# Performance work log

Measured on AMD Instinct MI355X. Metric: run time of the kernel, lower is better.

## Reference

```python
import jax, jax.numpy as jnp
import numpy as np

NUM_ANCHORS = 9  # 3 ratios * 3 sizes


def setup_inputs() -> dict:
    key = jax.random.key(0)
    k0, k1, k2, k3 = jax.random.split(key, 4)
    B, C, H, W = 4, 256, 200, 336
    resnet_features = jax.random.normal(k0, (B, C, H, W), dtype=jnp.float32)
    # 3x3 conv: C -> 512
    W1 = jax.random.normal(k1, (512, C, 3, 3), dtype=jnp.float32) * 0.02
    b1 = jnp.zeros((512,), dtype=jnp.float32)
    # 1x1 cls head: 512 -> 9*2
    Wc = jax.random.normal(k2, (NUM_ANCHORS * 2, 512), dtype=jnp.float32) * 0.02
    bc = jnp.zeros((NUM_ANCHORS * 2,), dtype=jnp.float32)
    # 1x1 bbox head: 512 -> 9*4
    Wb = jax.random.normal(k3, (NUM_ANCHORS * 4, 512), dtype=jnp.float32) * 0.02
    bb = jnp.zeros((NUM_ANCHORS * 4,), dtype=jnp.float32)
    return {"resnet_features": resnet_features, "W1": W1, "b1": b1,
            "Wc": Wc, "bc": bc, "Wb": Wb, "bb": bb}


def reference(resnet_features, W1, b1, Wc, bc, Wb, bb):
    B = resnet_features.shape[0]
    # conv3x3 + ReLU (padding=1 -> SAME)
    feat = jax.lax.conv_general_dilated(
        resnet_features, W1, window_strides=(1, 1), padding='SAME',
        dimension_numbers=('NCHW', 'OIHW', 'NCHW'))
    feat = jax.nn.relu(feat + b1[None, :, None, None])  # [B,512,H,W]
    # 1x1 conv heads as channel contractions
    cls = jnp.einsum('bchw,oc->bohw', feat, Wc) + bc[None, :, None, None]
    box = jnp.einsum('bchw,oc->bohw', feat, Wb) + bb[None, :, None, None]
    # permute(0,2,3,1).view(B,-1,2/4)
    anchor_cls_score = jnp.transpose(cls, (0, 2, 3, 1)).reshape(B, -1, 2)
    anchor_bboxdelta = jnp.transpose(box, (0, 2, 3, 1)).reshape(B, -1, 4)
    return anchor_cls_score, anchor_bboxdelta
```

## Files before the change

### kernel.cpp

```cpp
#include <hip/hip_runtime.h>
#include <hip/hip_bf16.h>
#include <stdint.h>

#define B_   4
#define C_   256
#define H_   200
#define W_   336
#define OC_  512
#define HP_  202
#define WP_  338
#define M_   (B_*H_*W_)
#define MTILES (M_/128)
#define OUT0_ (M_*18)
#define OUT_TOTAL_ (M_*54)

#define XP_ELEMS  ((size_t)B_*HP_*WP_*C_)
#define XP_BYTES  (XP_ELEMS*2)
#define W1T_ELEMS ((size_t)9*OC_*C_)
#define W1T_OFF   XP_BYTES
#define WHB_OFF   (W1T_OFF + W1T_ELEMS*2)

typedef unsigned short ushortT;
typedef __attribute__((ext_vector_type(8))) short bf16x8;
typedef __attribute__((ext_vector_type(4))) float f32x4;

static __device__ __forceinline__ ushortT f2bf(float x) {
    union { float f; uint32_t u; } v; v.f = x;
    uint32_t r = v.u + 0x7fff + ((v.u >> 16) & 1);
    return (ushortT)(r >> 16);
}

__global__ __launch_bounds__(256) void pad_transpose(const float* __restrict__ X,
                                                     ushortT* __restrict__ Xp) {
    int bid = blockIdx.x;
    int wc = bid % 6; int bh = bid / 6;
    int h = bh % H_;  int b = bh / H_;
    int w0 = wc * 64;
    int t = threadIdx.x;
    __shared__ ushortT tile[64 * 65];

    for (int c0 = 0; c0 < C_; c0 += 64) {
        if (c0) __syncthreads();
        int col  = t & 63;
        int rowb = t >> 6;
        #pragma unroll
        for (int rr = 0; rr < 16; ++rr) {
            int row = rowb * 16 + rr;
            int w = w0 + col;
            float val = 0.f;
            if (w < W_)
                val = X[(((size_t)(b*C_ + c0 + row))*H_ + h)*W_ + w];
            tile[row*65 + col] = f2bf(val);
        }
        __syncthreads();
        int pixel = t >> 2;
        int csub  = (t & 3) * 16;
        int w = w0 + pixel;
        if (w < W_) {
            union { ushortT u[16]; uint4 q[2]; } vals;
            #pragma unroll
            for (int j = 0; j < 16; ++j)
                vals.u[j] = tile[(csub + j)*65 + pixel];
            size_t dst = (((size_t)b*HP_ + (h+1))*WP_ + (w+1))*C_ + c0 + csub;
            *(uint4*)(Xp + dst)     = vals.q[0];
            *(uint4*)(Xp + dst + 8) = vals.q[1];
        }
    }
}

__global__ __launch_bounds__(256) void prep_w1(const float* __restrict__ W1,
                                               ushortT* __restrict__ W1t) {
    int t = blockIdx.x * 256 + threadIdx.x;
    if (t >= OC_*C_) return;
    const float* src = W1 + (size_t)t * 9;
    #pragma unroll
    for (int rs = 0; rs < 9; ++rs)
        W1t[(size_t)rs*OC_*C_ + t] = f2bf(src[rs]);
}

__global__ __launch_bounds__(256) void prep_whb(const float* __restrict__ Wc,
                                                const float* __restrict__ Wb,
                                                ushortT* __restrict__ Whb) {
    int t = blockIdx.x * 256 + threadIdx.x;
    if (t >= 64*512) return;
    int o = t >> 9, oc = t & 511;
    float v = 0.f;
    if (o < 18) v = Wc[o*512 + oc];
    else if (o < 54) v = Wb[(o-18)*512 + oc];
    Whb[t] = f2bf(v);
}

__global__ __launch_bounds__(256) void init_out(const float* __restrict__ bc,
                                                const float* __restrict__ bb,
                                                float* __restrict__ out) {
    int i = blockIdx.x * 256 + threadIdx.x;
    if (i < OUT0_) out[i] = bc[i % 18];
    else if (i < OUT_TOTAL_) out[i] = bb[(i - OUT0_) % 36];
}

#define FP_ 136

__global__ __launch_bounds__(256, 2) void conv_rpn(
    const ushortT* __restrict__ Xp, const ushortT* __restrict__ W1t,
    const float* __restrict__ b1,  const ushortT* __restrict__ Whb,
    float* __restrict__ out)
{
    __shared__ ushortT Asm[128*32];
    __shared__ ushortT Bsm[128*32];
    __shared__ ushortT Fsm[128*FP_];

    const int tid  = threadIdx.x;
    const int wave = tid >> 6;
    const int lane = tid & 63;
    const int col  = lane & 15;
    const int quad = lane >> 4;

    const int mtile = blockIdx.x >> 2;
    const int nblk  = blockIdx.x & 3;
    const int oc0   = nblk << 7;

    const int arow0 = wave*32 + (lane >> 2);
    const int csub  = (lane & 3) * 8;

    size_t pixbase[2];
    #pragma unroll
    for (int i = 0; i < 2; ++i) {
        int m = mtile*128 + arow0 + i*16;
        int b = m / (H_*W_);
        int rem = m % (H_*W_);
        int h = rem / W_;
        int w = rem % W_;
        pixbase[i] = (((size_t)b*HP_ + h)*WP_ + w)*C_ + csub;
    }
    const size_t bbase = ((size_t)(oc0 + arow0))*C_ + csub;

    f32x4 acc[4][4] = {};
    const int wm = (wave & 1) * 64;
    const int wn = (wave >> 1) * 64;

    for (int rs = 0; rs < 9; ++rs) {
        const int roff = ((rs/3)*WP_ + (rs%3)) * C_;
        const size_t wsrc = (size_t)rs*OC_*C_;
        for (int cs = 0; cs < C_; cs += 32) {
            __syncthreads();
            #pragma unroll
            for (int i = 0; i < 2; ++i) {
                const ushortT* g = Xp + pixbase[i] + roff + cs;
                ushortT* l = Asm + (wave*32 + i*16)*32;
                __builtin_amdgcn_global_load_lds(
                    (const __attribute__((address_space(1))) uint32_t*)g,
                    (__attribute__((address_space(3))) uint32_t*)l, 16, 0, 0);
            }
            #pragma unroll
            for (int i = 0; i < 2; ++i) {
                const ushortT* g = W1t + wsrc + bbase + (size_t)i*16*C_ + cs;
                ushortT* l = Bsm + (wave*32 + i*16)*32;
                __builtin_amdgcn_global_load_lds(
                    (const __attribute__((address_space(1))) uint32_t*)g,
                    (__attribute__((address_space(3))) uint32_t*)l, 16, 0, 0);
            }
            __syncthreads();

            bf16x8 af[4], bfr[4];
            #pragma unroll
            for (int mt = 0; mt < 4; ++mt)
                af[mt] = *(const bf16x8*)&Asm[(wm + mt*16 + col)*32 + quad*8];
            #pragma unroll
            for (int nt = 0; nt < 4; ++nt)
                bfr[nt] = *(const bf16x8*)&Bsm[(wn + nt*16 + col)*32 + quad*8];
            #pragma unroll
            for (int mt = 0; mt < 4; ++mt)
                #pragma unroll
                for (int nt = 0; nt < 4; ++nt)
                    acc[mt][nt] = __builtin_amdgcn_mfma_f32_16x16x32_bf16(
                        af[mt], bfr[nt], acc[mt][nt], 0, 0, 0);
        }
    }

    __syncthreads();
    float b1v[4];
    #pragma unroll
    for (int nt = 0; nt < 4; ++nt) b1v[nt] = b1[oc0 + wn + nt*16 + col];
    #pragma unroll
    for (int mt = 0; mt < 4; ++mt)
        #pragma unroll
        for (int nt = 0; nt < 4; ++nt)
            #pragma unroll
            for (int rg = 0; rg < 4; ++rg) {
                float v = acc[mt][nt][rg] + b1v[nt];
                v = fmaxf(v, 0.f);
                Fsm[(wm + mt*16 + quad*4 + rg)*FP_ + wn + nt*16 + col] = f2bf(v);
            }
    __syncthreads();

    f32x4 hacc[2][4] = {};
    #pragma unroll
    for (int ks = 0; ks < 4; ++ks) {
        bf16x8 ah[2];
        #pragma unroll
        for (int mt = 0; mt < 2; ++mt)
            ah[mt] = *(const bf16x8*)&Fsm[(wave*32 + mt*16 + col)*FP_ + ks*32 + quad*8];
        #pragma unroll
        for (int nt = 0; nt < 4; ++nt) {
            bf16x8 bh = *(const bf16x8*)&Whb[(nt*16 + col)*512 + oc0 + ks*32 + quad*8];
            #pragma unroll
            for (int mt = 0; mt < 2; ++mt)
                hacc[mt][nt] = __builtin_amdgcn_mfma_f32_16x16x32_bf16(
                    ah[mt], bh, hacc[mt][nt], 0, 0, 0);
        }
    }

    #pragma unroll
    for (int mt = 0; mt < 2; ++mt) {
        int mbase = mtile*128 + wave*32 + mt*16 + quad*4;
        #pragma unroll
        for (int nt = 0; nt < 4; ++nt) {
            int o = nt*16 + col;
            #pragma unroll
            for (int rg = 0; rg < 4; ++rg) {
                float v = hacc[mt][nt][rg];
                size_t p = (size_t)(mbase + rg);
                if (o < 18)      atomicAdd(out + p*18 + o, v);
                else if (o < 54) atomicAdd(out + OUT0_ + p*36 + (o - 18), v);
            }
        }
    }
}

extern "C" void kernel_launch(void* const* d_in, const int* in_sizes, int n_in,
                              void* d_out, int out_size, void* d_ws, size_t ws_size,
                              hipStream_t stream) {
    const float* X  = (const float*)d_in[0];
    const float* W1 = (const float*)d_in[1];
    const float* b1 = (const float*)d_in[2];
    const float* Wc = (const float*)d_in[3];
    const float* bc = (const float*)d_in[4];
    const float* Wb = (const float*)d_in[5];
    const float* bb = (const float*)d_in[6];
    float* out = (float*)d_out;

    ushortT* Xp  = (ushortT*)d_ws;
    ushortT* W1t = (ushortT*)((char*)d_ws + W1T_OFF);
    ushortT* Whb = (ushortT*)((char*)d_ws + WHB_OFF);

    hipMemsetAsync(d_ws, 0, XP_BYTES, stream);
    pad_transpose<<<B_*H_*6, 256, 0, stream>>>(X, Xp);
    prep_w1<<<(OC_*C_ + 255)/256, 256, 0, stream>>>(W1, W1t);
    prep_whb<<<(64*512 + 255)/256, 256, 0, stream>>>(Wc, Wb, Whb);
    init_out<<<(OUT_TOTAL_ + 255)/256, 256, 0, stream>>>(bc, bb, out);
    conv_rpn<<<MTILES*4, 256, 0, stream>>>(Xp, W1t, b1, Whb, out);
}
```

Measured before the change: 1.382 ms.

## Alias LDS, raise occupancy, swizzle LDS tiles, group blocks, zero only halo

Replaces the full memset of the padded input buffer with a small kernel that zeros only the one-pixel halo, since the interior is overwritten by pad_transpose anyway. The conv kernel now uses dynamic shared memory in which the epilogue buffer aliases the A/B staging tiles, and its launch bound rises to 4 blocks per CU to increase occupancy. It also applies an XOR swizzle to the 16-byte chunks written by global_load_lds and read by the MFMA fragments to cut LDS bank conflicts. Blocks are remapped so groups of 8 M-tiles share the 4 N-blocks, for better L2 reuse of input rows. The tighter register budget under 4 blocks per CU could cause spills.

```diff
diff --git a/kernel.cpp b/kernel.cpp
--- a/kernel.cpp
+++ b/kernel.cpp
@@ -30,6 +30,19 @@
     return (ushortT)(r >> 16);
 }
 
+__global__ __launch_bounds__(256) void zero_halo(ushortT* __restrict__ Xp) {
+    int i = blockIdx.x * 256 + threadIdx.x;
+    if (i >= 4 * 1076 * 32) return;
+    int pix = i >> 5, ch = (i & 31) * 8;
+    int b = pix / 1076, r = pix % 1076;
+    int h, w;
+    if (r < 338)      { h = 0;   w = r; }
+    else if (r < 676) { h = 201; w = r - 338; }
+    else { r -= 676; h = 1 + (r >> 1); w = (r & 1) ? 337 : 0; }
+    size_t dst = (((size_t)b*HP_ + h)*WP_ + w)*C_ + ch;
+    *(uint4*)(Xp + dst) = make_uint4(0, 0, 0, 0);
+}
+
 __global__ __launch_bounds__(256) void pad_transpose(const float* __restrict__ X,
                                                      ushortT* __restrict__ Xp) {
     int bid = blockIdx.x;
@@ -100,14 +113,18 @@
 
 #define FP_ 136
 
-__global__ __launch_bounds__(256, 2) void conv_rpn(
+#define GRID_GROUPS ((MTILES + 7) / 8)
+#define CONV_GRID   (GRID_GROUPS * 32)
+
+__global__ __launch_bounds__(256, 4) void conv_rpn(
     const ushortT* __restrict__ Xp, const ushortT* __restrict__ W1t,
     const float* __restrict__ b1,  const ushortT* __restrict__ Whb,
     float* __restrict__ out)
 {
-    __shared__ ushortT Asm[128*32];
-    __shared__ ushortT Bsm[128*32];
-    __shared__ ushortT Fsm[128*FP_];
+    extern __shared__ ushortT smem[];
+    ushortT* Asm = smem;
+    ushortT* Bsm = smem + 128*32;
+    ushortT* Fsm = smem;
 
     const int tid  = threadIdx.x;
     const int wave = tid >> 6;
@@ -115,12 +132,16 @@
     const int col  = lane & 15;
     const int quad = lane >> 4;
 
-    const int mtile = blockIdx.x >> 2;
-    const int nblk  = blockIdx.x & 3;
-    const int oc0   = nblk << 7;
+    const int bidx   = blockIdx.x;
+    const int grp    = bidx >> 5;
+    const int within = bidx & 31;
+    const int mtile  = grp * 8 + (within & 7);
+    const int nblk   = within >> 3;
+    if (mtile >= MTILES) return;
+    const int oc0 = nblk << 7;
 
     const int arow0 = wave*32 + (lane >> 2);
-    const int csub  = (lane & 3) * 8;
+    const int csub  = (((lane & 3) ^ ((lane >> 3) & 3)) * 8);
 
     size_t pixbase[2];
     #pragma unroll
@@ -137,6 +158,7 @@
     f32x4 acc[4][4] = {};
     const int wm = (wave & 1) * 64;
     const int wn = (wave >> 1) * 64;
+    const int swz = (quad ^ ((col >> 1) & 3)) * 8;
 
     for (int rs = 0; rs < 9; ++rs) {
         const int roff = ((rs/3)*WP_ + (rs%3)) * C_;
@@ -164,10 +186,10 @@
             bf16x8 af[4], bfr[4];
             #pragma unroll
             for (int mt = 0; mt < 4; ++mt)
-                af[mt] = *(const bf16x8*)&Asm[(wm + mt*16 + col)*32 + quad*8];
+                af[mt] = *(const bf16x8*)&Asm[(wm + mt*16 + col)*32 + swz];
             #pragma unroll
             for (int nt = 0; nt < 4; ++nt)
-                bfr[nt] = *(const bf16x8*)&Bsm[(wn + nt*16 + col)*32 + quad*8];
+                bfr[nt] = *(const bf16x8*)&Bsm[(wn + nt*16 + col)*32 + swz];
             #pragma unroll
             for (int mt = 0; mt < 4; ++mt)
                 #pragma unroll
@@ -243,10 +265,11 @@
     ushortT* W1t = (ushortT*)((char*)d_ws + W1T_OFF);
     ushortT* Whb = (ushortT*)((char*)d_ws + WHB_OFF);
 
-    hipMemsetAsync(d_ws, 0, XP_BYTES, stream);
+    zero_halo<<<(4*1076*32 + 255)/256, 256, 0, stream>>>(Xp);
     pad_transpose<<<B_*H_*6, 256, 0, stream>>>(X, Xp);
     prep_w1<<<(OC_*C_ + 255)/256, 256, 0, stream>>>(W1, W1t);
     prep_whb<<<(64*512 + 255)/256, 256, 0, stream>>>(Wc, Wb, Whb);
     init_out<<<(OUT_TOTAL_ + 255)/256, 256, 0, stream>>>(bc, bb, out);
-    conv_rpn<<<MTILES*4, 256, 0, stream>>>(Xp, W1t, b1, Whb, out);
-}
+    conv_rpn<<<CONV_GRID, 256, 128*FP_*sizeof(ushortT), stream>>>(
+        Xp, W1t, b1, Whb, out);
+}
```

New measurement: 1.208 ms. 1.14x faster.
